# Kernel tuning notes

Measured on AMD Instinct MI355X. Metric: run time of the kernel, lower is better.

Reference implementation:

```python
import jax, jax.numpy as jnp
import numpy as np

N = 50000
E = 800000
IN_DIM = 18
HID = 32
HEADS = 4
NEG_SLOPE = 0.2
LN_EPS = 1e-5


def setup_inputs() -> dict:
    key = jax.random.key(0)
    ks = jax.random.split(key, 16)
    def rn(k, shape, scale=0.1):
        return jax.random.normal(k, shape, dtype=jnp.float32) * scale
    inp = {}
    inp['x'] = jax.random.normal(ks[0], (N, IN_DIM), dtype=jnp.float32)
    inp['edge_index'] = jax.random.randint(ks[1], (2, E), 0, N)
    # layer dims: (in, heads, out, concat)
    dims = [(IN_DIM, HEADS, HID, True), (HID * HEADS, HEADS, HID, True), (HID * HEADS, 1, HID, False)]
    i = 2
    for l, (din, h, dout, concat) in enumerate(dims):
        inp[f'Wl{l}'] = rn(ks[i], (din, h * dout)); i += 1
        inp[f'bl{l}'] = jnp.zeros((h * dout,), jnp.float32)
        inp[f'Wr{l}'] = rn(ks[i], (din, h * dout)); i += 1
        inp[f'br{l}'] = jnp.zeros((h * dout,), jnp.float32)
        inp[f'att{l}'] = rn(ks[i], (h, dout)); i += 1
        ldim = h * dout if concat else dout
        inp[f'bo{l}'] = jnp.zeros((ldim,), jnp.float32)
        inp[f'g{l}'] = jnp.ones((ldim,), jnp.float32)
        inp[f'be{l}'] = jnp.zeros((ldim,), jnp.float32)
    inp['cW1'] = rn(ks[i], (HID, HID // 2)); i += 1
    inp['cb1'] = jnp.zeros((HID // 2,), jnp.float32)
    inp['cW2'] = rn(ks[i], (HID // 2, 1)); i += 1
    inp['cb2'] = jnp.zeros((1,), jnp.float32)
    return inp


def _layer_norm(h, g, b):
    mu = h.mean(-1, keepdims=True)
    var = h.var(-1, keepdims=True)
    return (h - mu) * jax.lax.rsqrt(var + LN_EPS) * g + b


def _gatv2(x, src, dst, Wl, bl, Wr, br, att, bo, heads, dout, concat):
    # PyG GATv2Conv (eval mode): x_j via lin_l (source), x_i via lin_r (target)
    n = x.shape[0]
    xl = (x @ Wl + bl).reshape(n, heads, dout)
    xr = (x @ Wr + br).reshape(n, heads, dout)
    e = jax.nn.leaky_relu(xl[src] + xr[dst], NEG_SLOPE)          # [E, H, D]
    logits = jnp.einsum('ehd,hd->eh', e, att)                    # [E, H]
    m = jax.ops.segment_max(logits, dst, num_segments=n)         # scatter-softmax over dst
    a = jnp.exp(logits - m[dst])
    denom = jax.ops.segment_sum(a, dst, num_segments=n)
    alpha = a / denom[dst]                                       # [E, H]
    out = jax.ops.segment_sum(xl[src] * alpha[:, :, None], dst, num_segments=n)
    out = out.reshape(n, heads * dout) if concat else out.mean(axis=1)
    return out + bo


def _forward(x, src, dst, params):
    h_in = x
    for (Wl, bl, Wr, br, att, bo, g, be, heads, dout, concat) in params[:-1]:
        pass
    layers = params
    for i, (Wl, bl, Wr, br, att, bo, g, be, heads, dout, concat) in enumerate(layers):
        h = _gatv2(h_in, src, dst, Wl, bl, Wr, br, att, bo, heads, dout, concat)
        h = jax.nn.elu(_layer_norm(h, g, be))
        if i > 0 and h.shape == h_in.shape:
            h = h + h_in
        h_in = h
    return h_in


def reference(x, edge_index, Wl0, bl0, Wr0, br0, att0, bo0, g0, be0,
              Wl1, bl1, Wr1, br1, att1, bo1, g1, be1,
              Wl2, bl2, Wr2, br2, att2, bo2, g2, be2,
              cW1, cb1, cW2, cb2):
    n = x.shape[0]
    loop = jnp.arange(n, dtype=edge_index.dtype)  # add_self_loops=True
    src = jnp.concatenate([edge_index[0], loop])
    dst = jnp.concatenate([edge_index[1], loop])
    params = [
        (Wl0, bl0, Wr0, br0, att0, bo0, g0, be0, HEADS, HID, True),
        (Wl1, bl1, Wr1, br1, att1, bo1, g1, be1, HEADS, HID, True),
        (Wl2, bl2, Wr2, br2, att2, bo2, g2, be2, 1, HID, False),
    ]
    h = _forward(x, src, dst, params)
    h = jax.nn.elu(h @ cW1 + cb1)
    out = (h @ cW2 + cb2).squeeze(-1)
    return out
```

## Files before the change

### kernel.cpp

```cpp
#include <hip/hip_runtime.h>
#include <math.h>

#define N_NODES 50000
#define N_EDGES 800000
#define ET (N_EDGES + N_NODES)


__global__ void k_init_deg(int* deg, int n) {
    int i = blockIdx.x * blockDim.x + threadIdx.x;
    if (i < n) deg[i] = 1;
}

__global__ void k_count(const int* __restrict__ dst, int* __restrict__ deg, int e) {
    int i = blockIdx.x * blockDim.x + threadIdx.x;
    if (i < e) atomicAdd(&deg[dst[i]], 1);
}

__global__ void k_scan(const int* __restrict__ deg, int* __restrict__ rowptr,
                       int* __restrict__ cursor, int n) {
    __shared__ int wsum[16];
    __shared__ int carry_sh;
    int t = threadIdx.x;
    int wid = t >> 6, lane = t & 63;
    if (t == 0) carry_sh = 0;
    __syncthreads();
    for (int base = 0; base < n; base += 1024) {
        int i = base + t;
        int v = (i < n) ? deg[i] : 0;
        int x = v;
#pragma unroll
        for (int off = 1; off < 64; off <<= 1) {
            int u = __shfl_up(x, off, 64);
            if (lane >= off) x += u;
        }
        if (lane == 63) wsum[wid] = x;
        __syncthreads();
        if (wid == 0) {
            int wv = (lane < 16) ? wsum[lane] : 0;
            int y = wv;
#pragma unroll
            for (int off = 1; off < 16; off <<= 1) {
                int u = __shfl_up(y, off, 64);
                if (lane >= off) y += u;
            }
            if (lane < 16) wsum[lane] = y - wv;
        }
        __syncthreads();
        int carry = carry_sh;
        int excl = carry + wsum[wid] + x - v;
        if (i < n) { rowptr[i] = excl; cursor[i] = excl; }
        __syncthreads();
        if (t == 1023) carry_sh = excl + v;
        __syncthreads();
    }
    if (t == 0) rowptr[n] = carry_sh;
}

__global__ void k_fill(const int* __restrict__ src, const int* __restrict__ dst,
                       int* __restrict__ cursor, int* __restrict__ csr_src) {
    int i = blockIdx.x * blockDim.x + threadIdx.x;
    if (i < N_EDGES) {
        int d = dst[i];
        int pos = atomicAdd(&cursor[d], 1);
        csr_src[pos] = src[i];
    } else if (i < ET) {
        int node = i - N_EDGES;
        int pos = atomicAdd(&cursor[node], 1);
        csr_src[pos] = node;
    }
}


__global__ void k_zero256(int* hist) { hist[threadIdx.x] = 0; }

__global__ void k_hist(const int* __restrict__ deg, int* __restrict__ hist, int n) {
    __shared__ int lh[256];
    lh[threadIdx.x] = 0;
    __syncthreads();
    for (int i = blockIdx.x * 256 + threadIdx.x; i < n; i += gridDim.x * 256) {
        int b = deg[i]; b = (b > 255) ? 255 : b;
        atomicAdd(&lh[b], 1);
    }
    __syncthreads();
    if (lh[threadIdx.x]) atomicAdd(&hist[threadIdx.x], lh[threadIdx.x]);
}

__global__ void k_binstart(const int* __restrict__ hist, int* __restrict__ bincur) {
    __shared__ int sh[256];
    int t = threadIdx.x;
    int v = hist[t];
    sh[t] = v;
    __syncthreads();
    for (int off = 1; off < 256; off <<= 1) {
        int u = (t >= off) ? sh[t - off] : 0;
        __syncthreads();
        sh[t] += u;
        __syncthreads();
    }
    bincur[t] = sh[t] - v;
}

__global__ void k_scatter(const int* __restrict__ deg, int* __restrict__ bincur,
                          int* __restrict__ order, int n) {
    __shared__ int lcount[256];
    __shared__ int lbase[256];
    int t = threadIdx.x;
    lcount[t] = 0;
    __syncthreads();
    int i = blockIdx.x * 256 + t;
    int b = 0, rank = 0;
    bool valid = (i < n);
    if (valid) {
        b = deg[i]; b = (b > 255) ? 255 : b;
        rank = atomicAdd(&lcount[b], 1);
    }
    __syncthreads();
    if (lcount[t] > 0) lbase[t] = atomicAdd(&bincur[t], lcount[t]);
    __syncthreads();
    if (valid) order[lbase[b] + rank] = i;
}


template<int K, int HD, int BN>
__global__ void k_gemm_t(const float* __restrict__ x,
                         const float* __restrict__ Wl, const float* __restrict__ bl,
                         const float* __restrict__ Wr, const float* __restrict__ br,
                         float* __restrict__ xl, float* __restrict__ xr, int n) {
    constexpr int BM = 64;
    constexpr int TM = 4;
    constexpr int TN = BN / 16;
    constexpr int CT_PER = HD / BN;
    __shared__ float xs[K][BM + 4];
    __shared__ float ws[K][BN];
    int m0 = blockIdx.x * BM;
    int ct = blockIdx.y;
    const float* W = (ct < CT_PER) ? Wl : Wr;
    const float* bias = (ct < CT_PER) ? bl : br;
    float* o = (ct < CT_PER) ? xl : xr;
    int colBase = (ct % CT_PER) * BN;
    int t = threadIdx.x;
    for (int i = t; i < BM * K; i += 256) {
        int r = i / K, c = i % K;
        xs[c][r] = (m0 + r < n) ? x[(size_t)(m0 + r) * K + c] : 0.f;
    }
    for (int i = t; i < K * BN; i += 256) {
        int r = i / BN, c = i % BN;
        ws[r][c] = W[r * HD + colBase + c];
    }
    __syncthreads();
    int tr = t / 16, tc = t % 16;
    float acc[TM][TN];
#pragma unroll
    for (int j = 0; j < TN; j++) {
        float bv = bias[colBase + tc * TN + j];
#pragma unroll
        for (int i = 0; i < TM; i++) acc[i][j] = bv;
    }
#pragma unroll 2
    for (int k = 0; k < K; k++) {
        float4 av = *(const float4*)&xs[k][tr * TM];
        float a[TM] = {av.x, av.y, av.z, av.w};
#pragma unroll
        for (int j = 0; j < TN; j++) {
            float bb = ws[k][tc * TN + j];
#pragma unroll
            for (int i = 0; i < TM; i++) acc[i][j] = fmaf(a[i], bb, acc[i][j]);
        }
    }
#pragma unroll
    for (int i = 0; i < TM; i++) {
        int r = m0 + tr * TM + i;
        if (r < n) {
#pragma unroll
            for (int j = 0; j < TN; j++)
                o[(size_t)r * HD + colBase + tc * TN + j] = acc[i][j];
        }
    }
}


template<int HD, int D, bool RES, bool CLS>
__global__ void k_gather_ln(const float* __restrict__ xl, const float* __restrict__ xr,
                            const float* __restrict__ att,
                            const int* __restrict__ rowptr, const int* __restrict__ csr_src,
                            const int* __restrict__ order,
                            const float* __restrict__ bo, const float* __restrict__ g,
                            const float* __restrict__ be, const float* res,
                            float* outh,
                            const float* cW1, const float* cb1,
                            const float* cW2, const float* cb2,
                            float* out, int n) {
    constexpr int VEC = 8;
    constexpr int L = HD / VEC;
    constexpr int NPW = 64 / L;
    constexpr int G = D / VEC;
    __shared__ float w1s[CLS ? 512 : 1];
    __shared__ float b1s[CLS ? 16 : 1];
    __shared__ float w2s[CLS ? 16 : 1];
    __shared__ float b2s[1];
    if (CLS) {
        int t = threadIdx.x;
        for (int i = t; i < 512; i += blockDim.x) w1s[i] = cW1[i];
        if (t < 16) { b1s[t] = cb1[t]; w2s[t] = cW2[t]; }
        if (t == 0) b2s[0] = cb2[0];
        __syncthreads();
    }
    int tid = blockIdx.x * blockDim.x + threadIdx.x;
    int wave = tid >> 6;
    int lane = tid & 63;
    int slot = wave * NPW + lane / L;
    if (slot >= n) return;
    int node = order[slot];
    int sub = lane % L;
    int f = sub * VEC;

    float xrv[8], attv[8], acc[8];
    {
        const float4* xrp = (const float4*)(xr + (size_t)node * HD + f);
        float4 a0 = xrp[0], a1 = xrp[1];
        xrv[0]=a0.x; xrv[1]=a0.y; xrv[2]=a0.z; xrv[3]=a0.w;
        xrv[4]=a1.x; xrv[5]=a1.y; xrv[6]=a1.z; xrv[7]=a1.w;
        const float4* ap = (const float4*)(att + f);
        float4 t0 = ap[0], t1 = ap[1];
        attv[0]=t0.x; attv[1]=t0.y; attv[2]=t0.z; attv[3]=t0.w;
        attv[4]=t1.x; attv[5]=t1.y; attv[6]=t1.z; attv[7]=t1.w;
#pragma unroll
        for (int i = 0; i < 8; i++) acc[i] = 0.f;
    }
    int e0 = rowptr[node];
    int deg = rowptr[node + 1] - e0;
    float m = -INFINITY, denom = 0.f;
    int s = csr_src[e0];
    const float4* xp = (const float4*)(xl + (size_t)s * HD + f);
    float4 u0 = xp[0], u1 = xp[1];
    for (int j = 0; j < deg; j++) {
        float4 c0 = u0, c1 = u1;
        if (j + 1 < deg) {
            int s2 = csr_src[e0 + j + 1];
            const float4* xp2 = (const float4*)(xl + (size_t)s2 * HD + f);
            u0 = xp2[0]; u1 = xp2[1];
        }
        float xlv[8] = {c0.x, c0.y, c0.z, c0.w, c1.x, c1.y, c1.z, c1.w};
        float part = 0.f;
#pragma unroll
        for (int i = 0; i < 8; i++) {
            float e = xlv[i] + xrv[i];
            e = (e > 0.f) ? e : 0.2f * e;
            part = fmaf(e, attv[i], part);
        }
#pragma unroll
        for (int msk = G / 2; msk >= 1; msk >>= 1) part += __shfl_xor(part, msk, 64);
        float nm = fmaxf(m, part);
        float sc = __expf(m - nm);
        float w  = __expf(part - nm);
        denom = fmaf(denom, sc, w);
#pragma unroll
        for (int i = 0; i < 8; i++) acc[i] = fmaf(acc[i], sc, w * xlv[i]);
        m = nm;
    }
    float inv = 1.f / denom;
    float v[8];
    float s1 = 0.f;
#pragma unroll
    for (int i = 0; i < 8; i++) {
        v[i] = acc[i] * inv + bo[f + i];
        s1 += v[i];
    }
#pragma unroll
    for (int msk = L / 2; msk >= 1; msk >>= 1) s1 += __shfl_xor(s1, msk, 64);
    float mu = s1 * (1.f / HD);
    float q = 0.f;
#pragma unroll
    for (int i = 0; i < 8; i++) { float d = v[i] - mu; q += d * d; }
#pragma unroll
    for (int msk = L / 2; msk >= 1; msk >>= 1) q += __shfl_xor(q, msk, 64);
    float rstd = rsqrtf(q * (1.f / HD) + 1e-5f);
    float y[8];
#pragma unroll
    for (int i = 0; i < 8; i++) {
        float t = (v[i] - mu) * rstd * g[f + i] + be[f + i];
        t = (t > 0.f) ? t : expm1f(t);
        if (RES) t += res[(size_t)node * HD + f + i];
        y[i] = t;
    }
    if constexpr (!CLS) {
        float4 o0 = {y[0], y[1], y[2], y[3]};
        float4 o1 = {y[4], y[5], y[6], y[7]};
        float4* op = (float4*)(outh + (size_t)node * HD + f);
        op[0] = o0; op[1] = o1;
    } else {
        float pj[16];
#pragma unroll
        for (int j = 0; j < 16; j++) pj[j] = 0.f;
#pragma unroll
        for (int k = 0; k < 8; k++) {
#pragma unroll
            for (int j = 0; j < 16; j++)
                pj[j] = fmaf(y[k], w1s[(f + k) * 16 + j], pj[j]);
        }
#pragma unroll
        for (int j = 0; j < 16; j++) {
            pj[j] += __shfl_xor(pj[j], 1, 64);
            pj[j] += __shfl_xor(pj[j], 2, 64);
        }
        float o = b2s[0];
#pragma unroll
        for (int j = 0; j < 16; j++) {
            float a2 = pj[j] + b1s[j];
            a2 = (a2 > 0.f) ? a2 : expm1f(a2);
            o = fmaf(a2, w2s[j], o);
        }
        if (sub == 0) out[node] = o;
    }
}


extern "C" void kernel_launch(void* const* d_in, const int* in_sizes, int n_in,
                              void* d_out, int out_size, void* d_ws, size_t ws_size,
                              hipStream_t stream) {
    (void)in_sizes; (void)n_in; (void)out_size; (void)ws_size;
    const float* x  = (const float*)d_in[0];
    const int*   ei = (const int*)d_in[1];
    const int* src = ei;
    const int* dst = ei + N_EDGES;

    const float* Wl0 = (const float*)d_in[2];
    const float* bl0 = (const float*)d_in[3];
    const float* Wr0 = (const float*)d_in[4];
    const float* br0 = (const float*)d_in[5];
    const float* att0= (const float*)d_in[6];
    const float* bo0 = (const float*)d_in[7];
    const float* g0  = (const float*)d_in[8];
    const float* be0 = (const float*)d_in[9];
    const float* Wl1 = (const float*)d_in[10];
    const float* bl1 = (const float*)d_in[11];
    const float* Wr1 = (const float*)d_in[12];
    const float* br1 = (const float*)d_in[13];
    const float* att1= (const float*)d_in[14];
    const float* bo1 = (const float*)d_in[15];
    const float* g1  = (const float*)d_in[16];
    const float* be1 = (const float*)d_in[17];
    const float* Wl2 = (const float*)d_in[18];
    const float* bl2 = (const float*)d_in[19];
    const float* Wr2 = (const float*)d_in[20];
    const float* br2 = (const float*)d_in[21];
    const float* att2= (const float*)d_in[22];
    const float* bo2 = (const float*)d_in[23];
    const float* g2  = (const float*)d_in[24];
    const float* be2 = (const float*)d_in[25];
    const float* cW1 = (const float*)d_in[26];
    const float* cb1 = (const float*)d_in[27];
    const float* cW2 = (const float*)d_in[28];
    const float* cb2 = (const float*)d_in[29];

    char* ws = (char*)d_ws;
    float* xl = (float*)ws; ws += (size_t)N_NODES * 128 * 4;
    float* xr = (float*)ws; ws += (size_t)N_NODES * 128 * 4;
    float* h0 = (float*)ws; ws += (size_t)N_NODES * 128 * 4;
    float* h1 = (float*)ws; ws += (size_t)N_NODES * 128 * 4;
    int* rowptr  = (int*)ws; ws += (size_t)(N_NODES + 1) * 4;
    int* cursor  = (int*)ws; ws += (size_t)N_NODES * 4;
    int* deg     = (int*)ws; ws += (size_t)N_NODES * 4;
    int* csr_src = (int*)ws; ws += (size_t)ET * 4;
    int* hist    = (int*)ws; ws += 256 * 4;
    int* bincur  = (int*)ws; ws += 256 * 4;
    int* order   = (int*)ws; ws += (size_t)N_NODES * 4;

    k_init_deg<<<(N_NODES + 255) / 256, 256, 0, stream>>>(deg, N_NODES);
    k_count<<<(N_EDGES + 255) / 256, 256, 0, stream>>>(dst, deg, N_EDGES);
    k_scan<<<1, 1024, 0, stream>>>(deg, rowptr, cursor, N_NODES);
    k_fill<<<(ET + 255) / 256, 256, 0, stream>>>(src, dst, cursor, csr_src);
    k_zero256<<<1, 256, 0, stream>>>(hist);
    k_hist<<<64, 256, 0, stream>>>(deg, hist, N_NODES);
    k_binstart<<<1, 256, 0, stream>>>(hist, bincur);
    k_scatter<<<(N_NODES + 255) / 256, 256, 0, stream>>>(deg, bincur, order, N_NODES);

    const int gx = (N_NODES + 63) / 64;
    const int gridG128 = (N_NODES + 15) / 16;
    const int gridG32  = (N_NODES + 63) / 64;

    k_gemm_t<18, 128, 64><<<dim3(gx, 4), 256, 0, stream>>>(x, Wl0, bl0, Wr0, br0, xl, xr, N_NODES);
    k_gather_ln<128, 32, false, false><<<gridG128, 256, 0, stream>>>(
        xl, xr, att0, rowptr, csr_src, order, bo0, g0, be0, nullptr, h0,
        nullptr, nullptr, nullptr, nullptr, nullptr, N_NODES);

    k_gemm_t<128, 128, 64><<<dim3(gx, 4), 256, 0, stream>>>(h0, Wl1, bl1, Wr1, br1, xl, xr, N_NODES);
    k_gather_ln<128, 32, true, false><<<gridG128, 256, 0, stream>>>(
        xl, xr, att1, rowptr, csr_src, order, bo1, g1, be1, h0, h1,
        nullptr, nullptr, nullptr, nullptr, nullptr, N_NODES);

    k_gemm_t<128, 32, 32><<<dim3(gx, 2), 256, 0, stream>>>(h1, Wl2, bl2, Wr2, br2, xl, xr, N_NODES);
    k_gather_ln<32, 32, false, true><<<gridG32, 256, 0, stream>>>(
        xl, xr, att2, rowptr, csr_src, order, bo2, g2, be2, nullptr, nullptr,
        cW1, cb1, cW2, cb2, (float*)d_out, N_NODES);
}
```

Before: 631.8 us.

## Retile node GEMMs with K-chunking, larger 8x8 register tiles and vector loads

The dense projection GEMM kernel now stages K in chunks (BK) through shared memory, uses 128-row blocks with 8x8 (or 8x2) register tiles per thread, and loads and stores with float4/float2. The goal is more compute per shared-memory read, less LDS footprint for K=128, and fewer global transactions. In exchange it uses more registers per thread under the new launch bounds. It also adds extra block syncs per K chunk and leaves fewer blocks in the grid. The float4 global loads of x assume rows are 16-byte aligned, which holds for K=128 but is not relied on for K=18 (the scalar path is used there).

```diff
diff --git a/kernel.cpp b/kernel.cpp
--- a/kernel.cpp
+++ b/kernel.cpp
@@ -121,59 +121,93 @@
 }
 
 
-template<int K, int HD, int BN>
+template<int K, int BK, int HD, int BN, int TM, int TN>
+__launch_bounds__(256, 4)
 __global__ void k_gemm_t(const float* __restrict__ x,
                          const float* __restrict__ Wl, const float* __restrict__ bl,
                          const float* __restrict__ Wr, const float* __restrict__ br,
                          float* __restrict__ xl, float* __restrict__ xr, int n) {
-    constexpr int BM = 64;
-    constexpr int TM = 4;
-    constexpr int TN = BN / 16;
+    constexpr int BM = 128;
     constexpr int CT_PER = HD / BN;
-    __shared__ float xs[K][BM + 4];
-    __shared__ float ws[K][BN];
+    __shared__ float xs[BK][BM + 4];
+    __shared__ float ws[BK][BN];
     int m0 = blockIdx.x * BM;
     int ct = blockIdx.y;
-    const float* W = (ct < CT_PER) ? Wl : Wr;
-    const float* bias = (ct < CT_PER) ? bl : br;
-    float* o = (ct < CT_PER) ? xl : xr;
+    const float* W  = (ct < CT_PER) ? Wl : Wr;
+    const float* bv = (ct < CT_PER) ? bl : br;
+    float* o        = (ct < CT_PER) ? xl : xr;
     int colBase = (ct % CT_PER) * BN;
     int t = threadIdx.x;
-    for (int i = t; i < BM * K; i += 256) {
-        int r = i / K, c = i % K;
-        xs[c][r] = (m0 + r < n) ? x[(size_t)(m0 + r) * K + c] : 0.f;
-    }
-    for (int i = t; i < K * BN; i += 256) {
-        int r = i / BN, c = i % BN;
-        ws[r][c] = W[r * HD + colBase + c];
-    }
-    __syncthreads();
-    int tr = t / 16, tc = t % 16;
+    int tr = t >> 4, tc = t & 15;
     float acc[TM][TN];
 #pragma unroll
     for (int j = 0; j < TN; j++) {
-        float bv = bias[colBase + tc * TN + j];
-#pragma unroll
-        for (int i = 0; i < TM; i++) acc[i][j] = bv;
-    }
+        float b0 = bv[colBase + tc * TN + j];
+#pragma unroll
+        for (int i = 0; i < TM; i++) acc[i][j] = b0;
+    }
+    for (int k0 = 0; k0 < K; k0 += BK) {
+        if constexpr ((BK % 4) == 0) {
+            constexpr int NFL4 = BM * BK / 4;
+            for (int idx = t; idx < NFL4; idx += 256) {
+                int r  = idx % BM;
+                int c0 = idx / BM;
+                float4 v = {0.f, 0.f, 0.f, 0.f};
+                int row = m0 + r;
+                if (row < n) v = *(const float4*)&x[(size_t)row * K + k0 + c0 * 4];
+                xs[c0 * 4 + 0][r] = v.x;
+                xs[c0 * 4 + 1][r] = v.y;
+                xs[c0 * 4 + 2][r] = v.z;
+                xs[c0 * 4 + 3][r] = v.w;
+            }
+        } else {
+            for (int idx = t; idx < BM * BK; idx += 256) {
+                int r = idx % BM;
+                int c = idx / BM;
+                float v = 0.f;
+                int row = m0 + r;
+                if (row < n) v = x[(size_t)row * K + k0 + c];
+                xs[c][r] = v;
+            }
+        }
+        for (int idx = t; idx < BK * BN; idx += 256) {
+            int r = idx / BN, c = idx % BN;
+            ws[r][c] = W[(size_t)(k0 + r) * HD + colBase + c];
+        }
+        __syncthreads();
 #pragma unroll 2
-    for (int k = 0; k < K; k++) {
-        float4 av = *(const float4*)&xs[k][tr * TM];
-        float a[TM] = {av.x, av.y, av.z, av.w};
-#pragma unroll
-        for (int j = 0; j < TN; j++) {
-            float bb = ws[k][tc * TN + j];
-#pragma unroll
-            for (int i = 0; i < TM; i++) acc[i][j] = fmaf(a[i], bb, acc[i][j]);
-        }
+        for (int k = 0; k < BK; k++) {
+            float a[TM], b[TN];
+#pragma unroll
+            for (int q = 0; q < TM; q += 4)
+                *(float4*)&a[q] = *(const float4*)&xs[k][tr * TM + q];
+            if constexpr (TN == 8) {
+                *(float4*)&b[0] = *(const float4*)&ws[k][tc * TN];
+                *(float4*)&b[4] = *(const float4*)&ws[k][tc * TN + 4];
+            } else if constexpr (TN == 4) {
+                *(float4*)&b[0] = *(const float4*)&ws[k][tc * TN];
+            } else {
+                *(float2*)&b[0] = *(const float2*)&ws[k][tc * TN];
+            }
+#pragma unroll
+            for (int i = 0; i < TM; i++)
+#pragma unroll
+                for (int j = 0; j < TN; j++)
+                    acc[i][j] = fmaf(a[i], b[j], acc[i][j]);
+        }
+        __syncthreads();
     }
 #pragma unroll
     for (int i = 0; i < TM; i++) {
         int r = m0 + tr * TM + i;
         if (r < n) {
-#pragma unroll
-            for (int j = 0; j < TN; j++)
-                o[(size_t)r * HD + colBase + tc * TN + j] = acc[i][j];
+            if constexpr ((TN % 4) == 0) {
+#pragma unroll
+                for (int j = 0; j < TN; j += 4)
+                    *(float4*)&o[(size_t)r * HD + colBase + tc * TN + j] = *(float4*)&acc[i][j];
+            } else {
+                *(float2*)&o[(size_t)r * HD + colBase + tc * TN] = *(float2*)&acc[i][0];
+            }
         }
     }
 }
@@ -375,21 +409,24 @@
     k_binstart<<<1, 256, 0, stream>>>(hist, bincur);
     k_scatter<<<(N_NODES + 255) / 256, 256, 0, stream>>>(deg, bincur, order, N_NODES);
 
-    const int gx = (N_NODES + 63) / 64;
+    const int gx128 = (N_NODES + 127) / 128;
     const int gridG128 = (N_NODES + 15) / 16;
     const int gridG32  = (N_NODES + 63) / 64;
 
-    k_gemm_t<18, 128, 64><<<dim3(gx, 4), 256, 0, stream>>>(x, Wl0, bl0, Wr0, br0, xl, xr, N_NODES);
+    k_gemm_t<18, 18, 128, 128, 8, 8><<<dim3(gx128, 2), 256, 0, stream>>>(
+        x, Wl0, bl0, Wr0, br0, xl, xr, N_NODES);
     k_gather_ln<128, 32, false, false><<<gridG128, 256, 0, stream>>>(
         xl, xr, att0, rowptr, csr_src, order, bo0, g0, be0, nullptr, h0,
         nullptr, nullptr, nullptr, nullptr, nullptr, N_NODES);
 
-    k_gemm_t<128, 128, 64><<<dim3(gx, 4), 256, 0, stream>>>(h0, Wl1, bl1, Wr1, br1, xl, xr, N_NODES);
+    k_gemm_t<128, 32, 128, 128, 8, 8><<<dim3(gx128, 2), 256, 0, stream>>>(
+        h0, Wl1, bl1, Wr1, br1, xl, xr, N_NODES);
     k_gather_ln<128, 32, true, false><<<gridG128, 256, 0, stream>>>(
         xl, xr, att1, rowptr, csr_src, order, bo1, g1, be1, h0, h1,
         nullptr, nullptr, nullptr, nullptr, nullptr, N_NODES);
 
-    k_gemm_t<128, 32, 32><<<dim3(gx, 2), 256, 0, stream>>>(h1, Wl2, bl2, Wr2, br2, xl, xr, N_NODES);
+    k_gemm_t<128, 32, 32, 32, 8, 2><<<dim3(gx128, 2), 256, 0, stream>>>(
+        h1, Wl2, bl2, Wr2, br2, xl, xr, N_NODES);
     k_gather_ln<32, 32, false, true><<<gridG32, 256, 0, stream>>>(
         xl, xr, att2, rowptr, csr_src, order, bo2, g2, be2, nullptr, nullptr,
         cW1, cb1, cW2, cb2, (float*)d_out, N_NODES);
```

Result: faster. 556.3 us (-12.0%).
